# Optimization experiments

Measured on AMD Instinct MI355X. Metric: run time of the kernel, lower is better.

Reference implementation:

```python
import jax, jax.numpy as jnp
from jax import lax
import numpy as np

N_IN = 4          # n_in_channels (WN input); coupling input has 2*N_IN channels
N_CTX = 80        # n_context_channels
N_LAYERS = 8
N_CH = 256        # n_channels (must be even)
K = 3             # kernel_size (odd)
DILATIONS = [1, 2, 4, 8, 16, 32, 64, 128]
B, T = 8, 4096


def conv1d(x, w, b, dilation=1):
    # x: [B, Cin, T], w: [Cout, Cin, K], 'same' padding as in the torch module
    pad = (w.shape[-1] * dilation - dilation) // 2
    y = lax.conv_general_dilated(
        x, w, window_strides=(1,), padding=[(pad, pad)],
        rhs_dilation=(dilation,), dimension_numbers=('NCH', 'OIH', 'NCH'))
    return y + b[None, :, None]


def setup_inputs() -> dict:
    key = jax.random.key(0)
    ks = jax.random.split(key, 14)
    s = 0.05  # weight scale to keep exp(log_s) well-conditioned
    inp = {
        'forecast': jax.random.normal(ks[0], (B, 2 * N_IN, T), jnp.float32),
        'context':  jax.random.normal(ks[1], (B, N_CTX, T), jnp.float32),
        'start_w': jax.random.normal(ks[2], (N_CH, N_IN, 1), jnp.float32) * s,
        'start_b': jax.random.normal(ks[3], (N_CH,), jnp.float32) * s,
        'cond_w':  jax.random.normal(ks[4], (2 * N_CH * N_LAYERS, N_CTX, 1), jnp.float32) * s,
        'cond_b':  jax.random.normal(ks[5], (2 * N_CH * N_LAYERS,), jnp.float32) * s,
        'in_w':    jax.random.normal(ks[6], (N_LAYERS, 2 * N_CH, N_CH, K), jnp.float32) * s,
        'in_b':    jax.random.normal(ks[7], (N_LAYERS, 2 * N_CH), jnp.float32) * s,
        # res_skip: layers 0..L-2 have 2*N_CH out channels; last layer uses only first N_CH
        'rs_w':    jax.random.normal(ks[8], (N_LAYERS, 2 * N_CH, N_CH, 1), jnp.float32) * s,
        'rs_b':    jax.random.normal(ks[9], (N_LAYERS, 2 * N_CH), jnp.float32) * s,
        'end_w':   jax.random.normal(ks[10], (2 * N_IN, N_CH, 1), jnp.float32) * 0.01,
        'end_b':   jax.random.normal(ks[11], (2 * N_IN,), jnp.float32) * 0.01,
    }
    return inp


def wn(f0, context, start_w, start_b, cond_w, cond_b, in_w, in_b, rs_w, rs_b, end_w, end_b):
    x = conv1d(f0, start_w, start_b)                 # [B, N_CH, T]
    ctx = conv1d(context, cond_w, cond_b)            # [B, 2*N_CH*L, T]
    output = jnp.zeros_like(x)
    for i in range(N_LAYERS):
        a = conv1d(x, in_w[i], in_b[i], DILATIONS[i])
        a = a + ctx[:, i * 2 * N_CH:(i + 1) * 2 * N_CH, :]
        acts = jnp.tanh(a[:, :N_CH, :]) * jax.nn.sigmoid(a[:, N_CH:, :])
        if i < N_LAYERS - 1:
            rs = conv1d(acts, rs_w[i], rs_b[i])      # [B, 2*N_CH, T]
            x = x + rs[:, :N_CH, :]
            output = output + rs[:, N_CH:, :]
        else:
            rs = conv1d(acts, rs_w[i][:N_CH], rs_b[i][:N_CH])
            output = output + rs
    return conv1d(output, end_w, end_b)              # [B, 2*N_IN, T]


def reference(forecast, context, start_w, start_b, cond_w, cond_b,
              in_w, in_b, rs_w, rs_b, end_w, end_b):
    n_half = forecast.shape[1] // 2
    f0 = forecast[:, :n_half, :]
    f1 = forecast[:, n_half:, :]
    out = wn(f0, context, start_w, start_b, cond_w, cond_b,
             in_w, in_b, rs_w, rs_b, end_w, end_b)
    log_s = out[:, n_half:, :]
    b = out[:, :n_half, :]
    f1 = jnp.exp(log_s) * f1 + b
    return jnp.concatenate([f0, f1], axis=1), log_s
```

## Files before the change

### kernel.cpp

```cpp
#include <hip/hip_runtime.h>

#define BATCH 8
#define T 4096
#define NCH 256
#define NCTX 80
#define NLAYERS 8

typedef unsigned short u16;
typedef __attribute__((ext_vector_type(8))) short short8;
typedef __attribute__((ext_vector_type(4))) short short4v;
typedef __attribute__((ext_vector_type(4))) float float4v;

__device__ __forceinline__ float b2f(u16 u) {
    unsigned v = ((unsigned)u) << 16;
    float f;
    __builtin_memcpy(&f, &v, 4);
    return f;
}
__device__ __forceinline__ u16 f2b(float f) {
    unsigned v;
    __builtin_memcpy(&v, &f, 4);
    unsigned r = v + 0x7FFFu + ((v >> 16) & 1u);
    return (u16)(r >> 16);
}

typedef const __attribute__((address_space(1))) unsigned int* gp1;
typedef __attribute__((address_space(3))) unsigned int* lp3;
__device__ __forceinline__ void gl_lds16(const u16* g, u16* l) {
    __builtin_amdgcn_global_load_lds((gp1)g, (lp3)l, 16, 0, 0);
}

__device__ __forceinline__ void wb0() { asm volatile("s_waitcnt vmcnt(0) lgkmcnt(0)\n\ts_barrier" ::: "memory"); }
__device__ __forceinline__ void wb4() { asm volatile("s_waitcnt vmcnt(4) lgkmcnt(0)\n\ts_barrier" ::: "memory"); }
__device__ __forceinline__ void wb5() { asm volatile("s_waitcnt vmcnt(5) lgkmcnt(0)\n\ts_barrier" ::: "memory"); }

template <bool F32>
__device__ __forceinline__ float LD(const void* p, size_t i) {
    if constexpr (F32) return ((const float*)p)[i];
    else return b2f(((const u16*)p)[i]);
}
template <bool F32>
__device__ __forceinline__ bool skipv(const int* flag) {
    int f = *flag;
    return F32 ? (f != 0) : (f == 0);
}

__global__ void probe_kernel(const u16* __restrict__ fc, int* __restrict__ flag) {
    __shared__ int cnt;
    if (threadIdx.x == 0) cnt = 0;
    __syncthreads();
    int local = 0;
#pragma unroll
    for (int j = 0; j < 16; j++) {
        u16 u = fc[2 * (threadIdx.x * 16 + j)];
        int e = (u >> 7) & 0xFF;
        if (e >= 0x50 && e <= 0x85) local++;
    }
    atomicAdd(&cnt, local);
    __syncthreads();
    if (threadIdx.x == 0) *flag = (cnt >= 2048) ? 1 : 0;
}

template <bool F32>
__global__ void cvt_kernel(const void* __restrict__ src, u16* __restrict__ dst, int n,
                           const int* __restrict__ flag) {
    if (skipv<F32>(flag)) return;
    int i = blockIdx.x * 256 + threadIdx.x;
    if (i < n) dst[i] = f2b(LD<F32>(src, i));
}

template <bool F32>
__global__ void prep_wc(const void* __restrict__ in_w, const void* __restrict__ in_b,
                        const void* __restrict__ cond_w, const void* __restrict__ cond_b,
                        u16* __restrict__ Wc, const int* __restrict__ flag) {
    if (skipv<F32>(flag)) return;
    int row = blockIdx.x;
    for (int it = 0; it < 4; it++) {
        int col = it * 256 + threadIdx.x;
        if (col >= 864) break;
        float v;
        if (col < 256)       v = LD<F32>(in_w, ((size_t)row * 256 + col) * 3);
        else if (col < 512)  v = LD<F32>(in_w, ((size_t)row * 256 + (col - 256)) * 3 + 1);
        else if (col < 768)  v = LD<F32>(in_w, ((size_t)row * 256 + (col - 512)) * 3 + 2);
        else if (col < 848)  v = LD<F32>(cond_w, (size_t)row * 80 + (col - 768));
        else if (col == 848) v = LD<F32>(in_b, row) + LD<F32>(cond_b, row);
        else                 v = 0.f;
        Wc[(size_t)row * 864 + col] = f2b(v);
    }
}

template <bool F32>
__global__ void prep_ctx(const void* __restrict__ ctx, u16* __restrict__ ctxt,
                         const int* __restrict__ flag) {
    if (skipv<F32>(flag)) return;
    __shared__ float sm[80][65];
    const int tid = threadIdx.x;
    const int b = blockIdx.y, t0 = blockIdx.x * 64;
    for (int it = 0; it < 20; it++) {
        int e = it * 256 + tid;
        int j = e >> 6, tt = e & 63;
        sm[j][tt] = LD<F32>(ctx, ((size_t)b * 80 + j) * T + t0 + tt);
    }
    __syncthreads();
    for (int it = 0; it < 24; it++) {
        int e = it * 256 + tid;
        int r = e / 96, c = e - r * 96;
        float v = (c < 80) ? sm[c][r] : (c == 80 ? 1.f : 0.f);
        ctxt[((size_t)b * T + t0 + r) * 96 + c] = f2b(v);
    }
}

template <bool F32>
__global__ void start_kernel(const void* __restrict__ fc, const void* __restrict__ w,
                             const void* __restrict__ bias, u16* __restrict__ xt,
                             const int* __restrict__ flag) {
    if (skipv<F32>(flag)) return;
    __shared__ float fsm[4][64];
    __shared__ float wsm[1024];
    __shared__ float bsm[256];
    const int tid = threadIdx.x;
    const int b = blockIdx.y, t0 = blockIdx.x * 64;
    fsm[tid >> 6][tid & 63] = LD<F32>(fc, ((size_t)b * 8 + (tid >> 6)) * T + t0 + (tid & 63));
    for (int it = 0; it < 4; it++) wsm[it * 256 + tid] = LD<F32>(w, it * 256 + tid);
    bsm[tid] = LD<F32>(bias, tid);
    __syncthreads();
    for (int r = 0; r < 64; r++) {
        int c = tid;
        float a = bsm[c];
#pragma unroll
        for (int k = 0; k < 4; k++) a += wsm[c * 4 + k] * fsm[k][r];
        xt[((size_t)b * T + t0 + r) * 256 + c] = f2b(a);
    }
}

__global__ __launch_bounds__(512, 1) void layer_conv(
    const u16* __restrict__ x, const u16* __restrict__ Wc, const u16* __restrict__ ctxt,
    u16* __restrict__ acts, int layer, int dil) {
    __shared__ u16 lds[61440];
    const int tid = threadIdx.x;
    const int w = tid >> 6, lane = tid & 63;
    const int l15 = lane & 15, quad = lane >> 4;
    const int iw = w >> 2, jc = w & 3;
    const int b = blockIdx.y, t0 = blockIdx.x * 128;
    const int lrow = lane >> 2;
    const int fw = (lrow ^ (lrow >> 2)) & 3;
    const int lsw = ((lane & 3) ^ fw) * 8;
    const int fr = (l15 ^ (l15 >> 2)) & 3;
    const int rq = (quad ^ fr) * 8;
    const int brb = 64 * (w >> 1) + 256 * (w & 1);

    const u16* xb = x + (size_t)b * T * 256;
    const u16* cb = ctxt + (size_t)b * T * 96;
    const u16* Wl = Wc + (size_t)layer * 512 * 864;

    float4v acc[4][8];
#pragma unroll
    for (int m = 0; m < 4; m++)
#pragma unroll
        for (int jj = 0; jj < 8; jj++) acc[m][jj] = (float4v){0.f, 0.f, 0.f, 0.f};

    auto stageA = [&](int s, int abuf) -> int {
        u16* dst = &lds[abuf * 4096 + w * 512];
        if (s < 24) {
            int seg = s >> 3, cs = s & 7;
            int tb = t0 + 16 * w + (seg - 1) * dil;
            if (tb >= 0 && tb + 16 <= T) {
                gl_lds16(xb + (size_t)(tb + lrow) * 256 + cs * 32 + lsw, dst);
                return 1;
            } else {
                int t = tb + lrow;
                short8 av = (short8){0, 0, 0, 0, 0, 0, 0, 0};
                if (t >= 0 && t < T)
                    av = *(const short8*)(xb + (size_t)t * 256 + cs * 32 + lsw);
                *(short4v*)&dst[lane * 8] = __builtin_shufflevector(av, av, 0, 1, 2, 3);
                *(short4v*)&dst[lane * 8 + 4] = __builtin_shufflevector(av, av, 4, 5, 6, 7);
                return 0;
            }
        } else {
            gl_lds16(cb + (size_t)(t0 + 16 * w + lrow) * 96 + (s - 24) * 32 + lsw, dst);
            return 1;
        }
    };
    auto stageB = [&](int s, int bbuf) {
        const u16* src = Wl + (size_t)(brb + lrow) * 864 + s * 32 + lsw;
        u16* dst = &lds[12288 + bbuf * 16384 + w * 2048];
        gl_lds16(src, dst);
        gl_lds16(src + (size_t)16 * 864, dst + 512);
        gl_lds16(src + (size_t)32 * 864, dst + 1024);
        gl_lds16(src + (size_t)48 * 864, dst + 1536);
    };

    int a0 = stageA(0, 0);
    stageB(0, 0);
    int a1 = stageA(1, 1);
    stageB(1, 1);
    (void)a0;
    if (a1) wb5(); else wb4();
#pragma unroll 1
    for (int s = 0; s < 27; s++) {
        int aiss = 0;
        if (s + 2 < 27) {
            aiss = stageA(s + 2, (s + 2) % 3);
            stageB(s + 2, (s + 2) % 3);
        }
        const u16* bA = &lds[(s % 3) * 4096];
        const u16* bB = &lds[12288 + (s % 3) * 16384];
        short8 af0 = *(const short8*)&bA[(64 * iw + l15) * 32 + rq];
        short8 af1 = *(const short8*)&bA[(64 * iw + 16 + l15) * 32 + rq];
        short8 af2 = *(const short8*)&bA[(64 * iw + 32 + l15) * 32 + rq];
        short8 af3 = *(const short8*)&bA[(64 * iw + 48 + l15) * 32 + rq];
        __builtin_amdgcn_s_setprio(1);
#pragma unroll
        for (int jj = 0; jj < 8; jj++) {
            short8 bf = *(const short8*)&bB[(128 * jc + 16 * jj + l15) * 32 + rq];
            acc[0][jj] = __builtin_amdgcn_mfma_f32_16x16x32_bf16(af0, bf, acc[0][jj], 0, 0, 0);
            acc[1][jj] = __builtin_amdgcn_mfma_f32_16x16x32_bf16(af1, bf, acc[1][jj], 0, 0, 0);
            acc[2][jj] = __builtin_amdgcn_mfma_f32_16x16x32_bf16(af2, bf, acc[2][jj], 0, 0, 0);
            acc[3][jj] = __builtin_amdgcn_mfma_f32_16x16x32_bf16(af3, bf, acc[3][jj], 0, 0, 0);
        }
        __builtin_amdgcn_s_setprio(0);
        if (s < 25) {
            if (aiss) wb5(); else wb4();
        } else if (s == 25) {
            wb0();
        }
    }

    u16* ab = acts + (size_t)b * T * 256;
#pragma unroll
    for (int m = 0; m < 4; m++)
#pragma unroll
        for (int jj = 0; jj < 4; jj++) {
            int o = 64 * jc + 16 * jj + l15;
#pragma unroll
            for (int r = 0; r < 4; r++) {
                int t = t0 + 64 * iw + 16 * m + quad * 4 + r;
                float at = acc[m][jj][r], as = acc[m][jj + 4][r];
                float e2 = __expf(2.f * at);
                float th = 1.f - 2.f / (e2 + 1.f);
                float sg = 1.f / (1.f + __expf(-as));
                ab[(size_t)t * 256 + o] = f2b(th * sg);
            }
        }
}

__global__ __launch_bounds__(512, 1) void layer_rs(
    const u16* __restrict__ acts, u16* __restrict__ x, const u16* __restrict__ Wrs,
    const u16* __restrict__ rsb, u16* __restrict__ oacc, int layer, int first, int last) {
    __shared__ u16 lds[61440];
    const int tid = threadIdx.x;
    const int w = tid >> 6, lane = tid & 63;
    const int l15 = lane & 15, quad = lane >> 4;
    const int iw = w >> 2, jc = w & 3;
    const int b = blockIdx.y, t0 = blockIdx.x * 128;
    const int lrow = lane >> 2;
    const int fw = (lrow ^ (lrow >> 2)) & 3;
    const int lsw = ((lane & 3) ^ fw) * 8;
    const int fr = (l15 ^ (l15 >> 2)) & 3;
    const int rq = (quad ^ fr) * 8;
    const int brb = 64 * (w >> 1) + 256 * (w & 1);

    const u16* ab = acts + (size_t)b * T * 256;
    const u16* Wr = Wrs + (size_t)layer * 512 * 256;

    float4v acc[4][8];
#pragma unroll
    for (int m = 0; m < 4; m++)
#pragma unroll
        for (int jj = 0; jj < 8; jj++) acc[m][jj] = (float4v){0.f, 0.f, 0.f, 0.f};

    auto stageA = [&](int s, int abuf) {
        gl_lds16(ab + (size_t)(t0 + 16 * w + lrow) * 256 + s * 32 + lsw,
                 &lds[abuf * 4096 + w * 512]);
    };
    auto stageB = [&](int s, int bbuf) {
        const u16* src = Wr + (size_t)(brb + lrow) * 256 + s * 32 + lsw;
        u16* dst = &lds[12288 + bbuf * 16384 + w * 2048];
        gl_lds16(src, dst);
        gl_lds16(src + (size_t)16 * 256, dst + 512);
        gl_lds16(src + (size_t)32 * 256, dst + 1024);
        gl_lds16(src + (size_t)48 * 256, dst + 1536);
    };

    stageA(0, 0);
    stageB(0, 0);
    stageA(1, 1);
    stageB(1, 1);
    wb5();
#pragma unroll 1
    for (int s = 0; s < 8; s++) {
        if (s + 2 < 8) {
            stageA(s + 2, (s + 2) % 3);
            stageB(s + 2, (s + 2) % 3);
        }
        const u16* bA = &lds[(s % 3) * 4096];
        const u16* bB = &lds[12288 + (s % 3) * 16384];
        short8 af0 = *(const short8*)&bA[(64 * iw + l15) * 32 + rq];
        short8 af1 = *(const short8*)&bA[(64 * iw + 16 + l15) * 32 + rq];
        short8 af2 = *(const short8*)&bA[(64 * iw + 32 + l15) * 32 + rq];
        short8 af3 = *(const short8*)&bA[(64 * iw + 48 + l15) * 32 + rq];
        __builtin_amdgcn_s_setprio(1);
#pragma unroll
        for (int jj = 0; jj < 8; jj++) {
            short8 bf = *(const short8*)&bB[(128 * jc + 16 * jj + l15) * 32 + rq];
            acc[0][jj] = __builtin_amdgcn_mfma_f32_16x16x32_bf16(af0, bf, acc[0][jj], 0, 0, 0);
            acc[1][jj] = __builtin_amdgcn_mfma_f32_16x16x32_bf16(af1, bf, acc[1][jj], 0, 0, 0);
            acc[2][jj] = __builtin_amdgcn_mfma_f32_16x16x32_bf16(af2, bf, acc[2][jj], 0, 0, 0);
            acc[3][jj] = __builtin_amdgcn_mfma_f32_16x16x32_bf16(af3, bf, acc[3][jj], 0, 0, 0);
        }
        __builtin_amdgcn_s_setprio(0);
        if (s < 6) wb5();
        else if (s == 6) wb0();
    }

    u16* xv = x + (size_t)b * T * 256;
    u16* oo = oacc + (size_t)b * T * 256;
#pragma unroll
    for (int m = 0; m < 4; m++)
#pragma unroll
        for (int jj = 0; jj < 8; jj++) {
            int o = 64 * jc + 16 * (jj & 3) + l15;
            if (jj < 4) {
                float b0 = b2f(rsb[layer * 512 + o]);
#pragma unroll
                for (int r = 0; r < 4; r++) {
                    int t = t0 + 64 * iw + 16 * m + quad * 4 + r;
                    size_t idx = (size_t)t * 256 + o;
                    float v0 = acc[m][jj][r] + b0;
                    if (last) oo[idx] = f2b(b2f(oo[idx]) + v0);
                    else      xv[idx] = f2b(b2f(xv[idx]) + v0);
                }
            } else if (!last) {
                float b1 = b2f(rsb[layer * 512 + 256 + o]);
#pragma unroll
                for (int r = 0; r < 4; r++) {
                    int t = t0 + 64 * iw + 16 * m + quad * 4 + r;
                    size_t idx = (size_t)t * 256 + o;
                    float v1 = acc[m][jj][r] + b1;
                    oo[idx] = first ? f2b(v1) : f2b(b2f(oo[idx]) + v1);
                }
            }
        }
}

template <bool F32>
__global__ void end_kernel(const u16* __restrict__ oacc, const void* __restrict__ w_end,
                           const void* __restrict__ b_end, const void* __restrict__ fc,
                           void* __restrict__ out, const int* __restrict__ flag) {
    if (skipv<F32>(flag)) return;
    __shared__ float wsm[2048];
    __shared__ float bsm[8];
    const int tid = threadIdx.x;
    for (int it = 0; it < 8; it++) wsm[it * 256 + tid] = LD<F32>(w_end, it * 256 + tid);
    if (tid < 8) bsm[tid] = LD<F32>(b_end, tid);
    __syncthreads();
    int gid = blockIdx.x * 256 + tid;
    int b = gid >> 12, t = gid & 4095;
    float o8[8];
#pragma unroll
    for (int o = 0; o < 8; o++) o8[o] = bsm[o];
    const u16* orow = oacc + (size_t)(b * T + t) * 256;
    for (int c8 = 0; c8 < 32; c8++) {
        short8 v8 = *(const short8*)(orow + c8 * 8);
#pragma unroll
        for (int k = 0; k < 8; k++) {
            float v = b2f((u16)v8[k]);
            int c = c8 * 8 + k;
#pragma unroll
            for (int o = 0; o < 8; o++) o8[o] += wsm[o * 256 + c] * v;
        }
    }
    size_t ob8 = (size_t)b * 8 * T;
#pragma unroll
    for (int j = 0; j < 4; j++) {
        float f1v = LD<F32>(fc, ob8 + (size_t)(4 + j) * T + t);
        float ls = o8[4 + j];
        float val = __expf(ls) * f1v + o8[j];
        if constexpr (F32) {
            float* o = (float*)out;
            o[ob8 + (size_t)j * T + t] = ((const float*)fc)[ob8 + (size_t)j * T + t];
            o[ob8 + (size_t)(4 + j) * T + t] = val;
            o[(size_t)BATCH * 8 * T + ((size_t)b * 4 + j) * T + t] = ls;
        } else {
            u16* o = (u16*)out;
            o[ob8 + (size_t)j * T + t] = ((const u16*)fc)[ob8 + (size_t)j * T + t];
            o[ob8 + (size_t)(4 + j) * T + t] = f2b(val);
            o[(size_t)BATCH * 8 * T + ((size_t)b * 4 + j) * T + t] = f2b(ls);
        }
    }
}

template <bool F32>
static void launch_prep(const void* forecast, const void* context, const void* start_w,
                        const void* start_b, const void* cond_w, const void* cond_b,
                        const void* in_w, const void* in_b, const void* rs_w, const void* rs_b,
                        u16* xA, u16* ctxt, u16* Wc, u16* Wrs, u16* rsb, const int* flag,
                        hipStream_t stream) {
    cvt_kernel<F32><<<4096, 256, 0, stream>>>(rs_w, Wrs, 8 * 512 * 256, flag);
    cvt_kernel<F32><<<16, 256, 0, stream>>>(rs_b, rsb, 4096, flag);
    prep_wc<F32><<<4096, 256, 0, stream>>>(in_w, in_b, cond_w, cond_b, Wc, flag);
    prep_ctx<F32><<<dim3(64, BATCH), 256, 0, stream>>>(context, ctxt, flag);
    start_kernel<F32><<<dim3(64, BATCH), 256, 0, stream>>>(forecast, start_w, start_b, xA, flag);
}

extern "C" void kernel_launch(void* const* d_in, const int* in_sizes, int n_in,
                              void* d_out, int out_size, void* d_ws, size_t ws_size,
                              hipStream_t stream) {
    const void* forecast = d_in[0];
    const void* context  = d_in[1];
    const void* start_w  = d_in[2];
    const void* start_b  = d_in[3];
    const void* cond_w   = d_in[4];
    const void* cond_b   = d_in[5];
    const void* in_w     = d_in[6];
    const void* in_b     = d_in[7];
    const void* rs_w     = d_in[8];
    const void* rs_b     = d_in[9];
    const void* end_w    = d_in[10];
    const void* end_b    = d_in[11];

    char* W = (char*)d_ws;
    int* flag = (int*)(W + 0);
    u16* xA   = (u16*)(W + 256);
    u16* oacc = (u16*)(W + 256 + 16777216);
    u16* acts = (u16*)(W + 256 + 33554432);
    u16* ctxt = (u16*)(W + 256 + 50331648);
    u16* Wc   = (u16*)(W + 256 + 56623104);
    u16* Wrs  = (u16*)(W + 256 + 63700992);
    u16* rsb  = (u16*)(W + 256 + 65798144);

    probe_kernel<<<1, 256, 0, stream>>>((const u16*)forecast, flag);

    launch_prep<false>(forecast, context, start_w, start_b, cond_w, cond_b, in_w, in_b, rs_w,
                       rs_b, xA, ctxt, Wc, Wrs, rsb, flag, stream);
    launch_prep<true>(forecast, context, start_w, start_b, cond_w, cond_b, in_w, in_b, rs_w,
                      rs_b, xA, ctxt, Wc, Wrs, rsb, flag, stream);

    const int dil[NLAYERS] = {1, 2, 4, 8, 16, 32, 64, 128};
    for (int l = 0; l < NLAYERS; l++) {
        layer_conv<<<dim3(32, BATCH), 512, 0, stream>>>(xA, Wc, ctxt, acts, l, dil[l]);
        layer_rs<<<dim3(32, BATCH), 512, 0, stream>>>(acts, xA, Wrs, rsb, oacc, l,
                                                      l == 0, l == NLAYERS - 1);
    }

    end_kernel<false><<<128, 256, 0, stream>>>(oacc, end_w, end_b, forecast, d_out, flag);
    end_kernel<true><<<128, 256, 0, stream>>>(oacc, end_w, end_b, forecast, d_out, flag);
}
```

Baseline: 683.3 us.

## Split layer kernels into 256-thread channel-half blocks for two blocks per CU

Layer conv and residual/skip kernels now launch twice as many 256-thread blocks, each computing half the output channels for a 128-timestep tile, with smaller LDS so two blocks can co-reside per CU. Per-wave stage loads are doubled to cover the full time tile, and the vmcnt wait thresholds are adjusted accordingly. The aim is better latency hiding and more independent scheduling than one 512-thread block per CU. The cost is that activation/input tiles are loaded twice, once per channel half.

Result: slower. 709.1 us (+3.8%).

```diff
diff --git a/kernel.cpp b/kernel.cpp
--- a/kernel.cpp
+++ b/kernel.cpp
@@ -33,6 +33,12 @@
 __device__ __forceinline__ void wb0() { asm volatile("s_waitcnt vmcnt(0) lgkmcnt(0)\n\ts_barrier" ::: "memory"); }
 __device__ __forceinline__ void wb4() { asm volatile("s_waitcnt vmcnt(4) lgkmcnt(0)\n\ts_barrier" ::: "memory"); }
 __device__ __forceinline__ void wb5() { asm volatile("s_waitcnt vmcnt(5) lgkmcnt(0)\n\ts_barrier" ::: "memory"); }
+__device__ __forceinline__ void wb6() { asm volatile("s_waitcnt vmcnt(6) lgkmcnt(0)\n\ts_barrier" ::: "memory"); }
+__device__ __forceinline__ void wbn(int n) {
+    if (n >= 6) wb6();
+    else if (n == 5) wb5();
+    else wb4();
+}
 
 template <bool F32>
 __device__ __forceinline__ float LD(const void* p, size_t i) {
@@ -133,21 +139,22 @@
     }
 }
 
-__global__ __launch_bounds__(512, 1) void layer_conv(
+__global__ __launch_bounds__(256, 2) void layer_conv(
     const u16* __restrict__ x, const u16* __restrict__ Wc, const u16* __restrict__ ctxt,
     u16* __restrict__ acts, int layer, int dil) {
-    __shared__ u16 lds[61440];
+    __shared__ u16 lds[36864];
     const int tid = threadIdx.x;
     const int w = tid >> 6, lane = tid & 63;
     const int l15 = lane & 15, quad = lane >> 4;
-    const int iw = w >> 2, jc = w & 3;
-    const int b = blockIdx.y, t0 = blockIdx.x * 128;
+    const int iw = w >> 1, jc = w & 1;
+    const int b = blockIdx.y;
+    const int cblk = blockIdx.x & 1, t0 = (blockIdx.x >> 1) * 128;
     const int lrow = lane >> 2;
     const int fw = (lrow ^ (lrow >> 2)) & 3;
     const int lsw = ((lane & 3) ^ fw) * 8;
     const int fr = (l15 ^ (l15 >> 2)) & 3;
     const int rq = (quad ^ fr) * 8;
-    const int brb = 64 * (w >> 1) + 256 * (w & 1);
+    const int brb = 128 * cblk + 64 * (w >> 1) + 256 * (w & 1);
 
     const u16* xb = x + (size_t)b * T * 256;
     const u16* cb = ctxt + (size_t)b * T * 96;
@@ -161,29 +168,36 @@
 
     auto stageA = [&](int s, int abuf) -> int {
         u16* dst = &lds[abuf * 4096 + w * 512];
+        int cnt = 0;
         if (s < 24) {
             int seg = s >> 3, cs = s & 7;
             int tb = t0 + 16 * w + (seg - 1) * dil;
-            if (tb >= 0 && tb + 16 <= T) {
-                gl_lds16(xb + (size_t)(tb + lrow) * 256 + cs * 32 + lsw, dst);
-                return 1;
-            } else {
-                int t = tb + lrow;
-                short8 av = (short8){0, 0, 0, 0, 0, 0, 0, 0};
-                if (t >= 0 && t < T)
-                    av = *(const short8*)(xb + (size_t)t * 256 + cs * 32 + lsw);
-                *(short4v*)&dst[lane * 8] = __builtin_shufflevector(av, av, 0, 1, 2, 3);
-                *(short4v*)&dst[lane * 8 + 4] = __builtin_shufflevector(av, av, 4, 5, 6, 7);
-                return 0;
+#pragma unroll
+            for (int h = 0; h < 2; h++) {
+                int tbh = tb + 64 * h;
+                u16* d = dst + 2048 * h;
+                if (tbh >= 0 && tbh + 16 <= T) {
+                    gl_lds16(xb + (size_t)(tbh + lrow) * 256 + cs * 32 + lsw, d);
+                    cnt++;
+                } else {
+                    int t = tbh + lrow;
+                    short8 av = (short8){0, 0, 0, 0, 0, 0, 0, 0};
+                    if (t >= 0 && t < T)
+                        av = *(const short8*)(xb + (size_t)t * 256 + cs * 32 + lsw);
+                    *(short4v*)&d[lane * 8] = __builtin_shufflevector(av, av, 0, 1, 2, 3);
+                    *(short4v*)&d[lane * 8 + 4] = __builtin_shufflevector(av, av, 4, 5, 6, 7);
+                }
             }
         } else {
             gl_lds16(cb + (size_t)(t0 + 16 * w + lrow) * 96 + (s - 24) * 32 + lsw, dst);
-            return 1;
-        }
+            gl_lds16(cb + (size_t)(t0 + 64 + 16 * w + lrow) * 96 + (s - 24) * 32 + lsw, dst + 2048);
+            cnt = 2;
+        }
+        return cnt;
     };
     auto stageB = [&](int s, int bbuf) {
         const u16* src = Wl + (size_t)(brb + lrow) * 864 + s * 32 + lsw;
-        u16* dst = &lds[12288 + bbuf * 16384 + w * 2048];
+        u16* dst = &lds[12288 + bbuf * 8192 + w * 2048];
         gl_lds16(src, dst);
         gl_lds16(src + (size_t)16 * 864, dst + 512);
         gl_lds16(src + (size_t)32 * 864, dst + 1024);
@@ -195,7 +209,7 @@
     int a1 = stageA(1, 1);
     stageB(1, 1);
     (void)a0;
-    if (a1) wb5(); else wb4();
+    wbn(4 + a1);
 #pragma unroll 1
     for (int s = 0; s < 27; s++) {
         int aiss = 0;
@@ -204,7 +218,7 @@
             stageB(s + 2, (s + 2) % 3);
         }
         const u16* bA = &lds[(s % 3) * 4096];
-        const u16* bB = &lds[12288 + (s % 3) * 16384];
+        const u16* bB = &lds[12288 + (s % 3) * 8192];
         short8 af0 = *(const short8*)&bA[(64 * iw + l15) * 32 + rq];
         short8 af1 = *(const short8*)&bA[(64 * iw + 16 + l15) * 32 + rq];
         short8 af2 = *(const short8*)&bA[(64 * iw + 32 + l15) * 32 + rq];
@@ -220,7 +234,7 @@
         }
         __builtin_amdgcn_s_setprio(0);
         if (s < 25) {
-            if (aiss) wb5(); else wb4();
+            wbn(4 + aiss);
         } else if (s == 25) {
             wb0();
         }
@@ -231,7 +245,7 @@
     for (int m = 0; m < 4; m++)
 #pragma unroll
         for (int jj = 0; jj < 4; jj++) {
-            int o = 64 * jc + 16 * jj + l15;
+            int o = 128 * cblk + 64 * jc + 16 * jj + l15;
 #pragma unroll
             for (int r = 0; r < 4; r++) {
                 int t = t0 + 64 * iw + 16 * m + quad * 4 + r;
@@ -244,21 +258,22 @@
         }
 }
 
-__global__ __launch_bounds__(512, 1) void layer_rs(
+__global__ __launch_bounds__(256, 2) void layer_rs(
     const u16* __restrict__ acts, u16* __restrict__ x, const u16* __restrict__ Wrs,
     const u16* __restrict__ rsb, u16* __restrict__ oacc, int layer, int first, int last) {
-    __shared__ u16 lds[61440];
+    __shared__ u16 lds[36864];
     const int tid = threadIdx.x;
     const int w = tid >> 6, lane = tid & 63;
     const int l15 = lane & 15, quad = lane >> 4;
-    const int iw = w >> 2, jc = w & 3;
-    const int b = blockIdx.y, t0 = blockIdx.x * 128;
+    const int iw = w >> 1, jc = w & 1;
+    const int b = blockIdx.y;
+    const int cblk = blockIdx.x & 1, t0 = (blockIdx.x >> 1) * 128;
     const int lrow = lane >> 2;
     const int fw = (lrow ^ (lrow >> 2)) & 3;
     const int lsw = ((lane & 3) ^ fw) * 8;
     const int fr = (l15 ^ (l15 >> 2)) & 3;
     const int rq = (quad ^ fr) * 8;
-    const int brb = 64 * (w >> 1) + 256 * (w & 1);
+    const int brb = 128 * cblk + 64 * (w >> 1) + 256 * (w & 1);
 
     const u16* ab = acts + (size_t)b * T * 256;
     const u16* Wr = Wrs + (size_t)layer * 512 * 256;
@@ -270,12 +285,13 @@
         for (int jj = 0; jj < 8; jj++) acc[m][jj] = (float4v){0.f, 0.f, 0.f, 0.f};
 
     auto stageA = [&](int s, int abuf) {
-        gl_lds16(ab + (size_t)(t0 + 16 * w + lrow) * 256 + s * 32 + lsw,
-                 &lds[abuf * 4096 + w * 512]);
+        u16* dst = &lds[abuf * 4096 + w * 512];
+        gl_lds16(ab + (size_t)(t0 + 16 * w + lrow) * 256 + s * 32 + lsw, dst);
+        gl_lds16(ab + (size_t)(t0 + 64 + 16 * w + lrow) * 256 + s * 32 + lsw, dst + 2048);
     };
     auto stageB = [&](int s, int bbuf) {
         const u16* src = Wr + (size_t)(brb + lrow) * 256 + s * 32 + lsw;
-        u16* dst = &lds[12288 + bbuf * 16384 + w * 2048];
+        u16* dst = &lds[12288 + bbuf * 8192 + w * 2048];
         gl_lds16(src, dst);
         gl_lds16(src + (size_t)16 * 256, dst + 512);
         gl_lds16(src + (size_t)32 * 256, dst + 1024);
@@ -286,7 +302,7 @@
     stageB(0, 0);
     stageA(1, 1);
     stageB(1, 1);
-    wb5();
+    wb6();
 #pragma unroll 1
     for (int s = 0; s < 8; s++) {
         if (s + 2 < 8) {
@@ -294,7 +310,7 @@
             stageB(s + 2, (s + 2) % 3);
         }
         const u16* bA = &lds[(s % 3) * 4096];
-        const u16* bB = &lds[12288 + (s % 3) * 16384];
+        const u16* bB = &lds[12288 + (s % 3) * 8192];
         short8 af0 = *(const short8*)&bA[(64 * iw + l15) * 32 + rq];
         short8 af1 = *(const short8*)&bA[(64 * iw + 16 + l15) * 32 + rq];
         short8 af2 = *(const short8*)&bA[(64 * iw + 32 + l15) * 32 + rq];
@@ -309,7 +325,7 @@
             acc[3][jj] = __builtin_amdgcn_mfma_f32_16x16x32_bf16(af3, bf, acc[3][jj], 0, 0, 0);
         }
         __builtin_amdgcn_s_setprio(0);
-        if (s < 6) wb5();
+        if (s < 6) wb6();
         else if (s == 6) wb0();
     }
 
@@ -319,7 +335,7 @@
     for (int m = 0; m < 4; m++)
 #pragma unroll
         for (int jj = 0; jj < 8; jj++) {
-            int o = 64 * jc + 16 * (jj & 3) + l15;
+            int o = 128 * cblk + 64 * jc + 16 * (jj & 3) + l15;
             if (jj < 4) {
                 float b0 = b2f(rsb[layer * 512 + o]);
 #pragma unroll
@@ -438,8 +454,8 @@
 
     const int dil[NLAYERS] = {1, 2, 4, 8, 16, 32, 64, 128};
     for (int l = 0; l < NLAYERS; l++) {
-        layer_conv<<<dim3(32, BATCH), 512, 0, stream>>>(xA, Wc, ctxt, acts, l, dil[l]);
-        layer_rs<<<dim3(32, BATCH), 512, 0, stream>>>(acts, xA, Wrs, rsb, oacc, l,
+        layer_conv<<<dim3(64, BATCH), 256, 0, stream>>>(xA, Wc, ctxt, acts, l, dil[l]);
+        layer_rs<<<dim3(64, BATCH), 256, 0, stream>>>(acts, xA, Wrs, rsb, oacc, l,
                                                       l == 0, l == NLAYERS - 1);
     }
 
```

## Switch GEMM pipelines to four-buffer double-step with one barrier per pair

Applied to the files above, without the earlier changes.

The conv and res-skip GEMM loops move from a triple-buffered pipeline with per-step partial vmcnt waits and barriers to a four-buffer scheme. Each iteration issues loads for two K-steps, computes two steps, then does a single full-drain wait plus barrier. This halves the barrier count and lets more loads be in flight per barrier. The cost is a larger LDS footprint (160 KB) and a full vmcnt(0) drain each iteration instead of overlapping the next prefetch.

Result: slower. 716.2 us (+4.8%).

```diff
diff --git a/kernel.cpp b/kernel.cpp
--- a/kernel.cpp
+++ b/kernel.cpp
@@ -30,9 +30,7 @@
     __builtin_amdgcn_global_load_lds((gp1)g, (lp3)l, 16, 0, 0);
 }
 
-__device__ __forceinline__ void wb0() { asm volatile("s_waitcnt vmcnt(0) lgkmcnt(0)\n\ts_barrier" ::: "memory"); }
-__device__ __forceinline__ void wb4() { asm volatile("s_waitcnt vmcnt(4) lgkmcnt(0)\n\ts_barrier" ::: "memory"); }
-__device__ __forceinline__ void wb5() { asm volatile("s_waitcnt vmcnt(5) lgkmcnt(0)\n\ts_barrier" ::: "memory"); }
+__device__ __forceinline__ void wbar() { asm volatile("s_waitcnt vmcnt(0) lgkmcnt(0)\n\ts_barrier" ::: "memory"); }
 
 template <bool F32>
 __device__ __forceinline__ float LD(const void* p, size_t i) {
@@ -136,7 +134,7 @@
 __global__ __launch_bounds__(512, 1) void layer_conv(
     const u16* __restrict__ x, const u16* __restrict__ Wc, const u16* __restrict__ ctxt,
     u16* __restrict__ acts, int layer, int dil) {
-    __shared__ u16 lds[61440];
+    __shared__ u16 lds[81920];
     const int tid = threadIdx.x;
     const int w = tid >> 6, lane = tid & 63;
     const int l15 = lane & 15, quad = lane >> 4;
@@ -159,14 +157,13 @@
 #pragma unroll
         for (int jj = 0; jj < 8; jj++) acc[m][jj] = (float4v){0.f, 0.f, 0.f, 0.f};
 
-    auto stageA = [&](int s, int abuf) -> int {
-        u16* dst = &lds[abuf * 4096 + w * 512];
+    auto stageA = [&](int s) {
+        u16* dst = &lds[(s & 3) * 4096 + w * 512];
         if (s < 24) {
             int seg = s >> 3, cs = s & 7;
             int tb = t0 + 16 * w + (seg - 1) * dil;
             if (tb >= 0 && tb + 16 <= T) {
                 gl_lds16(xb + (size_t)(tb + lrow) * 256 + cs * 32 + lsw, dst);
-                return 1;
             } else {
                 int t = tb + lrow;
                 short8 av = (short8){0, 0, 0, 0, 0, 0, 0, 0};
@@ -174,37 +171,22 @@
                     av = *(const short8*)(xb + (size_t)t * 256 + cs * 32 + lsw);
                 *(short4v*)&dst[lane * 8] = __builtin_shufflevector(av, av, 0, 1, 2, 3);
                 *(short4v*)&dst[lane * 8 + 4] = __builtin_shufflevector(av, av, 4, 5, 6, 7);
-                return 0;
             }
         } else {
             gl_lds16(cb + (size_t)(t0 + 16 * w + lrow) * 96 + (s - 24) * 32 + lsw, dst);
-            return 1;
-        }
-    };
-    auto stageB = [&](int s, int bbuf) {
+        }
+    };
+    auto stageB = [&](int s) {
         const u16* src = Wl + (size_t)(brb + lrow) * 864 + s * 32 + lsw;
-        u16* dst = &lds[12288 + bbuf * 16384 + w * 2048];
+        u16* dst = &lds[16384 + (s & 3) * 16384 + w * 2048];
         gl_lds16(src, dst);
         gl_lds16(src + (size_t)16 * 864, dst + 512);
         gl_lds16(src + (size_t)32 * 864, dst + 1024);
         gl_lds16(src + (size_t)48 * 864, dst + 1536);
     };
-
-    int a0 = stageA(0, 0);
-    stageB(0, 0);
-    int a1 = stageA(1, 1);
-    stageB(1, 1);
-    (void)a0;
-    if (a1) wb5(); else wb4();
-#pragma unroll 1
-    for (int s = 0; s < 27; s++) {
-        int aiss = 0;
-        if (s + 2 < 27) {
-            aiss = stageA(s + 2, (s + 2) % 3);
-            stageB(s + 2, (s + 2) % 3);
-        }
-        const u16* bA = &lds[(s % 3) * 4096];
-        const u16* bB = &lds[12288 + (s % 3) * 16384];
+    auto compute = [&](int s) {
+        const u16* bA = &lds[(s & 3) * 4096];
+        const u16* bB = &lds[16384 + (s & 3) * 16384];
         short8 af0 = *(const short8*)&bA[(64 * iw + l15) * 32 + rq];
         short8 af1 = *(const short8*)&bA[(64 * iw + 16 + l15) * 32 + rq];
         short8 af2 = *(const short8*)&bA[(64 * iw + 32 + l15) * 32 + rq];
@@ -219,12 +201,27 @@
             acc[3][jj] = __builtin_amdgcn_mfma_f32_16x16x32_bf16(af3, bf, acc[3][jj], 0, 0, 0);
         }
         __builtin_amdgcn_s_setprio(0);
-        if (s < 25) {
-            if (aiss) wb5(); else wb4();
-        } else if (s == 25) {
-            wb0();
-        }
-    }
+    };
+
+    stageA(0);
+    stageB(0);
+    stageA(1);
+    stageB(1);
+    wbar();
+#pragma unroll 1
+    for (int i = 0; i < 13; i++) {
+        int s2 = 2 * i + 2, s3 = 2 * i + 3;
+        stageA(s2);
+        stageB(s2);
+        if (s3 < 27) {
+            stageA(s3);
+            stageB(s3);
+        }
+        compute(2 * i);
+        compute(2 * i + 1);
+        wbar();
+    }
+    compute(26);
 
     u16* ab = acts + (size_t)b * T * 256;
 #pragma unroll
@@ -247,7 +244,7 @@
 __global__ __launch_bounds__(512, 1) void layer_rs(
     const u16* __restrict__ acts, u16* __restrict__ x, const u16* __restrict__ Wrs,
     const u16* __restrict__ rsb, u16* __restrict__ oacc, int layer, int first, int last) {
-    __shared__ u16 lds[61440];
+    __shared__ u16 lds[81920];
     const int tid = threadIdx.x;
     const int w = tid >> 6, lane = tid & 63;
     const int l15 = lane & 15, quad = lane >> 4;
@@ -269,32 +266,21 @@
 #pragma unroll
         for (int jj = 0; jj < 8; jj++) acc[m][jj] = (float4v){0.f, 0.f, 0.f, 0.f};
 
-    auto stageA = [&](int s, int abuf) {
+    auto stageA = [&](int s) {
         gl_lds16(ab + (size_t)(t0 + 16 * w + lrow) * 256 + s * 32 + lsw,
-                 &lds[abuf * 4096 + w * 512]);
-    };
-    auto stageB = [&](int s, int bbuf) {
+                 &lds[(s & 3) * 4096 + w * 512]);
+    };
+    auto stageB = [&](int s) {
         const u16* src = Wr + (size_t)(brb + lrow) * 256 + s * 32 + lsw;
-        u16* dst = &lds[12288 + bbuf * 16384 + w * 2048];
+        u16* dst = &lds[16384 + (s & 3) * 16384 + w * 2048];
         gl_lds16(src, dst);
         gl_lds16(src + (size_t)16 * 256, dst + 512);
         gl_lds16(src + (size_t)32 * 256, dst + 1024);
         gl_lds16(src + (size_t)48 * 256, dst + 1536);
     };
-
-    stageA(0, 0);
-    stageB(0, 0);
-    stageA(1, 1);
-    stageB(1, 1);
-    wb5();
-#pragma unroll 1
-    for (int s = 0; s < 8; s++) {
-        if (s + 2 < 8) {
-            stageA(s + 2, (s + 2) % 3);
-            stageB(s + 2, (s + 2) % 3);
-        }
-        const u16* bA = &lds[(s % 3) * 4096];
-        const u16* bB = &lds[12288 + (s % 3) * 16384];
+    auto compute = [&](int s) {
+        const u16* bA = &lds[(s & 3) * 4096];
+        const u16* bB = &lds[16384 + (s & 3) * 16384];
         short8 af0 = *(const short8*)&bA[(64 * iw + l15) * 32 + rq];
         short8 af1 = *(const short8*)&bA[(64 * iw + 16 + l15) * 32 + rq];
         short8 af2 = *(const short8*)&bA[(64 * iw + 32 + l15) * 32 + rq];
@@ -309,8 +295,25 @@
             acc[3][jj] = __builtin_amdgcn_mfma_f32_16x16x32_bf16(af3, bf, acc[3][jj], 0, 0, 0);
         }
         __builtin_amdgcn_s_setprio(0);
-        if (s < 6) wb5();
-        else if (s == 6) wb0();
+    };
+
+    stageA(0);
+    stageB(0);
+    stageA(1);
+    stageB(1);
+    wbar();
+#pragma unroll 1
+    for (int i = 0; i < 4; i++) {
+        int s2 = 2 * i + 2, s3 = 2 * i + 3;
+        if (s2 < 8) {
+            stageA(s2);
+            stageB(s2);
+            stageA(s3);
+            stageB(s3);
+        }
+        compute(2 * i);
+        compute(2 * i + 1);
+        if (i < 3) wbar();
     }
 
     u16* xv = x + (size_t)b * T * 256;
```

## Fuse dilated conv and res/skip GEMM into one kernel via LDS-resident activations

Applied to the files above, without the earlier changes.

Merges layer_conv and layer_rs into a single kernel per layer. The gated tanh*sigmoid activations are written into a swizzled LDS tile and consumed directly by the res/skip MFMA GEMM, so the per-layer acts buffer no longer makes a round trip through global memory and one launch per layer disappears. Because other blocks read neighbouring time steps of x through the dilation halo, x is now ping-ponged between two buffers so no block overwrites input another block still needs. The kernel uses more LDS (160KB), which removes any headroom for co-residency, and the second GEMM cannot start until the first one has fully drained.

Result: slower. 728.4 us (+6.6%).

```diff
diff --git a/kernel.cpp b/kernel.cpp
--- a/kernel.cpp
+++ b/kernel.cpp
@@ -33,6 +33,7 @@
 __device__ __forceinline__ void wb0() { asm volatile("s_waitcnt vmcnt(0) lgkmcnt(0)\n\ts_barrier" ::: "memory"); }
 __device__ __forceinline__ void wb4() { asm volatile("s_waitcnt vmcnt(4) lgkmcnt(0)\n\ts_barrier" ::: "memory"); }
 __device__ __forceinline__ void wb5() { asm volatile("s_waitcnt vmcnt(5) lgkmcnt(0)\n\ts_barrier" ::: "memory"); }
+__device__ __forceinline__ void wbar() { asm volatile("s_waitcnt vmcnt(0) lgkmcnt(0)\n\ts_barrier" ::: "memory"); }
 
 template <bool F32>
 __device__ __forceinline__ float LD(const void* p, size_t i) {
@@ -133,10 +134,11 @@
     }
 }
 
-__global__ __launch_bounds__(512, 1) void layer_conv(
-    const u16* __restrict__ x, const u16* __restrict__ Wc, const u16* __restrict__ ctxt,
-    u16* __restrict__ acts, int layer, int dil) {
-    __shared__ u16 lds[61440];
+__global__ __launch_bounds__(512, 1) void layer_fused(
+    const u16* __restrict__ xin, u16* __restrict__ xout, const u16* __restrict__ Wc,
+    const u16* __restrict__ ctxt, const u16* __restrict__ Wrs, const u16* __restrict__ rsb,
+    u16* __restrict__ oacc, int layer, int dil, int first, int last) {
+    __shared__ u16 lds[81920];
     const int tid = threadIdx.x;
     const int w = tid >> 6, lane = tid & 63;
     const int l15 = lane & 15, quad = lane >> 4;
@@ -149,9 +151,10 @@
     const int rq = (quad ^ fr) * 8;
     const int brb = 64 * (w >> 1) + 256 * (w & 1);
 
-    const u16* xb = x + (size_t)b * T * 256;
+    const u16* xb = xin + (size_t)b * T * 256;
     const u16* cb = ctxt + (size_t)b * T * 96;
     const u16* Wl = Wc + (size_t)layer * 512 * 864;
+    const u16* Wr = Wrs + (size_t)layer * 512 * 256;
 
     float4v acc[4][8];
 #pragma unroll
@@ -225,95 +228,66 @@
             wb0();
         }
     }
-
-    u16* ab = acts + (size_t)b * T * 256;
-#pragma unroll
-    for (int m = 0; m < 4; m++)
-#pragma unroll
-        for (int jj = 0; jj < 4; jj++) {
-            int o = 64 * jc + 16 * jj + l15;
-#pragma unroll
-            for (int r = 0; r < 4; r++) {
-                int t = t0 + 64 * iw + 16 * m + quad * 4 + r;
-                float at = acc[m][jj][r], as = acc[m][jj + 4][r];
-                float e2 = __expf(2.f * at);
-                float th = 1.f - 2.f / (e2 + 1.f);
-                float sg = 1.f / (1.f + __expf(-as));
-                ab[(size_t)t * 256 + o] = f2b(th * sg);
-            }
-        }
-}
-
-__global__ __launch_bounds__(512, 1) void layer_rs(
-    const u16* __restrict__ acts, u16* __restrict__ x, const u16* __restrict__ Wrs,
-    const u16* __restrict__ rsb, u16* __restrict__ oacc, int layer, int first, int last) {
-    __shared__ u16 lds[61440];
-    const int tid = threadIdx.x;
-    const int w = tid >> 6, lane = tid & 63;
-    const int l15 = lane & 15, quad = lane >> 4;
-    const int iw = w >> 2, jc = w & 3;
-    const int b = blockIdx.y, t0 = blockIdx.x * 128;
-    const int lrow = lane >> 2;
-    const int fw = (lrow ^ (lrow >> 2)) & 3;
-    const int lsw = ((lane & 3) ^ fw) * 8;
-    const int fr = (l15 ^ (l15 >> 2)) & 3;
-    const int rq = (quad ^ fr) * 8;
-    const int brb = 64 * (w >> 1) + 256 * (w & 1);
-
-    const u16* ab = acts + (size_t)b * T * 256;
-    const u16* Wr = Wrs + (size_t)layer * 512 * 256;
-
-    float4v acc[4][8];
-#pragma unroll
-    for (int m = 0; m < 4; m++)
-#pragma unroll
-        for (int jj = 0; jj < 8; jj++) acc[m][jj] = (float4v){0.f, 0.f, 0.f, 0.f};
-
-    auto stageA = [&](int s, int abuf) {
-        gl_lds16(ab + (size_t)(t0 + 16 * w + lrow) * 256 + s * 32 + lsw,
-                 &lds[abuf * 4096 + w * 512]);
-    };
-    auto stageB = [&](int s, int bbuf) {
+    __syncthreads();
+
+    auto stageBr = [&](int s) {
         const u16* src = Wr + (size_t)(brb + lrow) * 256 + s * 32 + lsw;
-        u16* dst = &lds[12288 + bbuf * 16384 + w * 2048];
+        u16* dst = &lds[32768 + (s % 3) * 16384 + w * 2048];
         gl_lds16(src, dst);
         gl_lds16(src + (size_t)16 * 256, dst + 512);
         gl_lds16(src + (size_t)32 * 256, dst + 1024);
         gl_lds16(src + (size_t)48 * 256, dst + 1536);
     };
-
-    stageA(0, 0);
-    stageB(0, 0);
-    stageA(1, 1);
-    stageB(1, 1);
-    wb5();
+    stageBr(0);
+    stageBr(1);
+
+#pragma unroll
+    for (int m = 0; m < 4; m++)
+#pragma unroll
+        for (int jj = 0; jj < 4; jj++) {
+            int col = 64 * jc + 16 * jj + l15;
+            int ch = col >> 3, co = col & 7;
+#pragma unroll
+            for (int r = 0; r < 4; r++) {
+                int row = 64 * iw + 16 * m + quad * 4 + r;
+                float at = acc[m][jj][r], as = acc[m][jj + 4][r];
+                float e2 = __expf(2.f * at);
+                float th = 1.f - 2.f / (e2 + 1.f);
+                float sg = 1.f / (1.f + __expf(-as));
+                lds[row * 256 + ((ch ^ (row & 7)) << 3) + co] = f2b(th * sg);
+            }
+        }
+    wbar();
+
+    float4v racc[4][8];
+#pragma unroll
+    for (int m = 0; m < 4; m++)
+#pragma unroll
+        for (int jj = 0; jj < 8; jj++) racc[m][jj] = (float4v){0.f, 0.f, 0.f, 0.f};
 #pragma unroll 1
     for (int s = 0; s < 8; s++) {
-        if (s + 2 < 8) {
-            stageA(s + 2, (s + 2) % 3);
-            stageB(s + 2, (s + 2) % 3);
-        }
-        const u16* bA = &lds[(s % 3) * 4096];
-        const u16* bB = &lds[12288 + (s % 3) * 16384];
-        short8 af0 = *(const short8*)&bA[(64 * iw + l15) * 32 + rq];
-        short8 af1 = *(const short8*)&bA[(64 * iw + 16 + l15) * 32 + rq];
-        short8 af2 = *(const short8*)&bA[(64 * iw + 32 + l15) * 32 + rq];
-        short8 af3 = *(const short8*)&bA[(64 * iw + 48 + l15) * 32 + rq];
+        if (s + 2 < 8) stageBr(s + 2);
+        const u16* bB = &lds[32768 + (s % 3) * 16384];
+        short8 raf0 = *(const short8*)&lds[(64 * iw + l15) * 256 + (((4 * s + quad) ^ (l15 & 7)) << 3)];
+        short8 raf1 = *(const short8*)&lds[(64 * iw + 16 + l15) * 256 + (((4 * s + quad) ^ (l15 & 7)) << 3)];
+        short8 raf2 = *(const short8*)&lds[(64 * iw + 32 + l15) * 256 + (((4 * s + quad) ^ (l15 & 7)) << 3)];
+        short8 raf3 = *(const short8*)&lds[(64 * iw + 48 + l15) * 256 + (((4 * s + quad) ^ (l15 & 7)) << 3)];
         __builtin_amdgcn_s_setprio(1);
 #pragma unroll
         for (int jj = 0; jj < 8; jj++) {
             short8 bf = *(const short8*)&bB[(128 * jc + 16 * jj + l15) * 32 + rq];
-            acc[0][jj] = __builtin_amdgcn_mfma_f32_16x16x32_bf16(af0, bf, acc[0][jj], 0, 0, 0);
-            acc[1][jj] = __builtin_amdgcn_mfma_f32_16x16x32_bf16(af1, bf, acc[1][jj], 0, 0, 0);
-            acc[2][jj] = __builtin_amdgcn_mfma_f32_16x16x32_bf16(af2, bf, acc[2][jj], 0, 0, 0);
-            acc[3][jj] = __builtin_amdgcn_mfma_f32_16x16x32_bf16(af3, bf, acc[3][jj], 0, 0, 0);
+            racc[0][jj] = __builtin_amdgcn_mfma_f32_16x16x32_bf16(raf0, bf, racc[0][jj], 0, 0, 0);
+            racc[1][jj] = __builtin_amdgcn_mfma_f32_16x16x32_bf16(raf1, bf, racc[1][jj], 0, 0, 0);
+            racc[2][jj] = __builtin_amdgcn_mfma_f32_16x16x32_bf16(raf2, bf, racc[2][jj], 0, 0, 0);
+            racc[3][jj] = __builtin_amdgcn_mfma_f32_16x16x32_bf16(raf3, bf, racc[3][jj], 0, 0, 0);
         }
         __builtin_amdgcn_s_setprio(0);
-        if (s < 6) wb5();
+        if (s < 6) wb4();
         else if (s == 6) wb0();
     }
 
-    u16* xv = x + (size_t)b * T * 256;
+    const u16* xi = xin + (size_t)b * T * 256;
+    u16* xo = xout + (size_t)b * T * 256;
     u16* oo = oacc + (size_t)b * T * 256;
 #pragma unroll
     for (int m = 0; m < 4; m++)
@@ -326,9 +300,9 @@
                 for (int r = 0; r < 4; r++) {
                     int t = t0 + 64 * iw + 16 * m + quad * 4 + r;
                     size_t idx = (size_t)t * 256 + o;
-                    float v0 = acc[m][jj][r] + b0;
+                    float v0 = racc[m][jj][r] + b0;
                     if (last) oo[idx] = f2b(b2f(oo[idx]) + v0);
-                    else      xv[idx] = f2b(b2f(xv[idx]) + v0);
+                    else      xo[idx] = f2b(b2f(xi[idx]) + v0);
                 }
             } else if (!last) {
                 float b1 = b2f(rsb[layer * 512 + 256 + o]);
@@ -336,7 +310,7 @@
                 for (int r = 0; r < 4; r++) {
                     int t = t0 + 64 * iw + 16 * m + quad * 4 + r;
                     size_t idx = (size_t)t * 256 + o;
-                    float v1 = acc[m][jj][r] + b1;
+                    float v1 = racc[m][jj][r] + b1;
                     oo[idx] = first ? f2b(v1) : f2b(b2f(oo[idx]) + v1);
                 }
             }
@@ -423,7 +397,7 @@
     int* flag = (int*)(W + 0);
     u16* xA   = (u16*)(W + 256);
     u16* oacc = (u16*)(W + 256 + 16777216);
-    u16* acts = (u16*)(W + 256 + 33554432);
+    u16* xB   = (u16*)(W + 256 + 33554432);
     u16* ctxt = (u16*)(W + 256 + 50331648);
     u16* Wc   = (u16*)(W + 256 + 56623104);
     u16* Wrs  = (u16*)(W + 256 + 63700992);
@@ -438,9 +412,10 @@
 
     const int dil[NLAYERS] = {1, 2, 4, 8, 16, 32, 64, 128};
     for (int l = 0; l < NLAYERS; l++) {
-        layer_conv<<<dim3(32, BATCH), 512, 0, stream>>>(xA, Wc, ctxt, acts, l, dil[l]);
-        layer_rs<<<dim3(32, BATCH), 512, 0, stream>>>(acts, xA, Wrs, rsb, oacc, l,
-                                                      l == 0, l == NLAYERS - 1);
+        u16* xin  = (l & 1) ? xB : xA;
+        u16* xout = (l & 1) ? xA : xB;
+        layer_fused<<<dim3(32, BATCH), 512, 0, stream>>>(xin, xout, Wc, ctxt, Wrs, rsb, oacc,
+                                                         l, dil[l], l == 0, l == NLAYERS - 1);
     }
 
     end_kernel<false><<<128, 256, 0, stream>>>(oacc, end_w, end_b, forecast, d_out, flag);
```
